# Kernel optimization log

Measured on AMD Instinct MI355X. Metric: run time of the kernel, lower is better.

Reference implementation:

```python
import jax, jax.numpy as jnp
import numpy as np


def _conv(x, w):
    # stride-2, pad-1, 3x3 conv, NCHW activations, HWIO kernel
    return jax.lax.conv_general_dilated(
        x, w, (2, 2), [(1, 1), (1, 1)],
        dimension_numbers=('NCHW', 'HWIO', 'NCHW'))


def setup_inputs() -> dict:
    key = jax.random.key(0)
    ks = iter(jax.random.split(key, 40))
    def rn(shape, scale=1.0):
        return jax.random.normal(next(ks), shape, jnp.float32) * scale
    d = {}
    d['img'] = rn((64, 3, 128, 128))
    d['qst'] = rn((64, 128))
    d['conv_w0'] = rn((3, 3, 3, 24), 1.0 / np.sqrt(3 * 9))
    for i in (1, 2, 3):
        d['conv_w%d' % i] = rn((3, 3, 24, 24), 1.0 / np.sqrt(24 * 9))
    for i in range(4):
        d['bn_s%d' % i] = jax.random.uniform(next(ks), (24,), jnp.float32, 0.5, 1.5)
        d['bn_b%d' % i] = rn((24,), 0.1)
    d['g_w1'] = rn((180, 256), 1.0 / np.sqrt(180))
    d['g_b1'] = rn((256,), 0.01)
    for i in (2, 3, 4):
        d['g_w%d' % i] = rn((256, 256), 1.0 / np.sqrt(256))
        d['g_b%d' % i] = rn((256,), 0.01)
    d['f_w1'] = rn((256, 256), 1.0 / np.sqrt(256))
    d['f_b1'] = rn((256,), 0.01)
    d['f_w2'] = rn((256, 256), 1.0 / np.sqrt(256))
    d['f_b2'] = rn((256,), 0.01)
    d['cls_w'] = rn((256, 32), 1.0 / np.sqrt(256))
    d['cls_b'] = rn((32,), 0.01)
    return d


def reference(img, qst, conv_w0, conv_w1, conv_w2, conv_w3,
              bn_s0, bn_b0, bn_s1, bn_b1, bn_s2, bn_b2, bn_s3, bn_b3,
              g_w1, g_b1, g_w2, g_b2, g_w3, g_b3, g_w4, g_b4,
              f_w1, f_b1, f_w2, f_b2, cls_w, cls_b):
    x = img
    for w, s, b in ((conv_w0, bn_s0, bn_b0), (conv_w1, bn_s1, bn_b1),
                    (conv_w2, bn_s2, bn_b2), (conv_w3, bn_s3, bn_b3)):
        x = jax.nn.relu(_conv(x, w) * s[None, :, None, None] + b[None, :, None, None])
    N, C, H, W = x.shape  # [64, 24, 8, 8]
    # positional encoding: coords_x, coords_y in [-1,1]
    cx, cy = jnp.meshgrid(jnp.linspace(-1.0, 1.0, W), jnp.linspace(-1.0, 1.0, H))
    pos = jnp.broadcast_to(jnp.stack([cx, cy])[None], (N, 2, H, W)).astype(x.dtype)
    x = jnp.concatenate([x, pos], axis=1)              # [N, C+2, H, W]
    Cf = C + 2
    x = x.transpose(0, 2, 3, 1).reshape(N, H * W, Cf)  # [N, HW, 26]
    # RN_G first linear decomposed over concat([x_i, x_j, qst]) so the huge
    # [N, HW, HW, 2C+q] concat tensor is never materialized (same math).
    W1a, W1b, W1c = g_w1[:Cf], g_w1[Cf:2 * Cf], g_w1[2 * Cf:]
    hi = x @ W1a                      # [N, HW, 256]
    hj = x @ W1b                      # [N, HW, 256]
    hq = qst @ W1c + g_b1             # [N, 256]
    h = jax.nn.relu(hi[:, :, None, :] + hj[:, None, :, :] + hq[:, None, None, :])  # [N,HW,HW,256]
    h = jax.nn.relu(h @ g_w2 + g_b2)
    h = jax.nn.relu(h @ g_w3 + g_b3)
    h = jax.nn.relu(h @ g_w4 + g_b4)
    s = h.sum(axis=(1, 2))            # sum over all HW*HW pairs -> [N, 256]
    # RN_F (dropout is identity in eval mode)
    y = jax.nn.relu(s @ f_w1 + f_b1)
    y = jax.nn.relu(y @ f_w2 + f_b2)
    return jax.nn.log_softmax(y @ cls_w + cls_b, axis=1)
```

## Files before the change

kernel.cpp:

```cpp
#include <hip/hip_runtime.h>
#include <hip/hip_bf16.h>
#include <math.h>

typedef __bf16 bf16x8 __attribute__((ext_vector_type(8)));
typedef __bf16 bf16x4 __attribute__((ext_vector_type(4)));
typedef float  f32x4  __attribute__((ext_vector_type(4)));

#define LH 264

__global__ __launch_bounds__(256) void k1(const float* __restrict__ img, const float* __restrict__ w0,
    const float* __restrict__ bs0, const float* __restrict__ bb0,
    const float* __restrict__ g2, const float* __restrict__ g3, const float* __restrict__ g4,
    const float* __restrict__ gw1, const float* __restrict__ gb1, const float* __restrict__ qst,
    float* __restrict__ c0, __bf16* __restrict__ Wt, float* __restrict__ hq,
    float* __restrict__ sbuf) {
  __shared__ __align__(16) float smem[8224];
  const int blk = blockIdx.x, t = threadIdx.x;

  if (blk < 512) {
    float* wl = smem;
    for (int i = t; i < 648; i += 256) wl[i] = w0[i];
    __syncthreads();
    const int H = 128, W = 128, OH = 64, OW = 64;
    int idx = blk * 256 + t;
    int oxh = idx & 31; int tt = idx >> 5; int oy = tt & 63; int n = tt >> 6;
    int ox0 = oxh * 2;
    float acc0[24], acc1[24];
#pragma unroll
    for (int co = 0; co < 24; ++co) { acc0[co] = 0.f; acc1[co] = 0.f; }
    for (int ci = 0; ci < 3; ++ci) {
      const float* xp = img + (size_t)(n * 3 + ci) * H * W;
#pragma unroll
      for (int ky = 0; ky < 3; ++ky) {
        int iy = 2 * oy + ky - 1;
        if (iy < 0 || iy >= H) continue;
        const float* row = xp + (size_t)iy * W;
        int ixb = 2 * ox0 - 1;
        float in[7];
#pragma unroll
        for (int u = 0; u < 7; ++u) {
          int ix = ixb + u;
          in[u] = (ix >= 0 && ix < W) ? row[ix] : 0.f;
        }
#pragma unroll
        for (int kx = 0; kx < 3; ++kx) {
          const float* wp = &wl[((ky * 3 + kx) * 3 + ci) * 24];
          float v0 = in[kx], v1 = in[kx + 2];
#pragma unroll
          for (int co = 0; co < 24; ++co) {
            float wv = wp[co];
            acc0[co] += v0 * wv;
            acc1[co] += v1 * wv;
          }
        }
      }
    }
    float* yp = c0 + (size_t)n * 24 * OH * OW + (size_t)oy * OW + ox0;
#pragma unroll
    for (int co = 0; co < 24; ++co) {
      float s = bs0[co], b = bb0[co];
      yp[(size_t)co * OH * OW]     = fmaxf(acc0[co] * s + b, 0.f);
      yp[(size_t)co * OH * OW + 1] = fmaxf(acc1[co] * s + b, 0.f);
    }
  } else if (blk < 536) {
    float* tile = smem;
    const int lb = blk - 512;
    const int l = lb >> 3, ks = lb & 7;
    const float* src = (l == 0) ? g2 : (l == 1) ? g3 : g4;
    for (int kk = 0; kk < 32; ++kk) tile[kk * 257 + t] = src[(ks * 32 + kk) * 256 + t];
    __syncthreads();
    const int q = t & 3, nb = t >> 2;
    __bf16* out = Wt + (size_t)(l * 8 + ks) * 8192;
#pragma unroll
    for (int i = 0; i < 4; ++i) {
      int nn = i * 64 + nb;
      bf16x8 v;
#pragma unroll
      for (int j = 0; j < 8; ++j) v[j] = (__bf16)tile[(q * 8 + j) * 257 + nn];
      *(bf16x8*)&out[nn * 32 + q * 8] = v;
    }
  } else {
    float* qs = smem;
    const int n = blk - 536;
    sbuf[n * 256 + t] = 0.f;
    if (t < 128) qs[t] = qst[n * 128 + t];
    __syncthreads();
    float a = gb1[t];
    for (int c = 0; c < 128; ++c) a += qs[c] * gw1[(52 + c) * 256 + t];
    hq[n * 256 + t] = a;
  }
}

__global__ __launch_bounds__(256) void conv1_k(const float* __restrict__ x, const float* __restrict__ w,
                                               const float* __restrict__ sc, const float* __restrict__ bi,
                                               float* __restrict__ y) {
  const int H = 64, W = 64, OH = 32, OW = 32;
  __shared__ float wl[2592];
  const int half = blockIdx.x & 1, sb = blockIdx.x >> 1;
  for (int i = threadIdx.x; i < 2592; i += 256) {
    int co = i % 12, rest = i / 12;
    wl[i] = w[rest * 24 + half * 12 + co];
  }
  __syncthreads();

  int idx = sb * 256 + threadIdx.x;
  int oxh = idx & 15; int tt = idx >> 4; int oy = tt & 31; int n = tt >> 5;
  int ox0 = oxh * 2;

  float acc0[12], acc1[12];
#pragma unroll
  for (int co = 0; co < 12; ++co) { acc0[co] = 0.f; acc1[co] = 0.f; }

  for (int ci = 0; ci < 24; ++ci) {
    const float* xp = x + (size_t)(n * 24 + ci) * H * W;
#pragma unroll
    for (int ky = 0; ky < 3; ++ky) {
      int iy = 2 * oy + ky - 1;
      if (iy < 0 || iy >= H) continue;
      const float* row = xp + (size_t)iy * W;
      int ixb = 2 * ox0 - 1;
      float in[7];
#pragma unroll
      for (int u = 0; u < 7; ++u) {
        int ix = ixb + u;
        in[u] = (ix >= 0 && ix < W) ? row[ix] : 0.f;
      }
#pragma unroll
      for (int kx = 0; kx < 3; ++kx) {
        const float* wp = &wl[((ky * 3 + kx) * 24 + ci) * 12];
        float v0 = in[kx], v1 = in[kx + 2];
#pragma unroll
        for (int co = 0; co < 12; ++co) {
          float wv = wp[co];
          acc0[co] += v0 * wv;
          acc1[co] += v1 * wv;
        }
      }
    }
  }
  float* yp = y + (size_t)n * 24 * OH * OW + (size_t)(half * 12) * OH * OW + (size_t)oy * OW + ox0;
#pragma unroll
  for (int co = 0; co < 12; ++co) {
    int cog = half * 12 + co;
    float s = sc[cog], b = bi[cog];
    yp[(size_t)co * OH * OW]     = fmaxf(acc0[co] * s + b, 0.f);
    yp[(size_t)co * OH * OW + 1] = fmaxf(acc1[co] * s + b, 0.f);
  }
}

__global__ __launch_bounds__(256) void chain2_k(const float* __restrict__ c1,
    const float* __restrict__ w2, const float* __restrict__ bs2, const float* __restrict__ bb2,
    const float* __restrict__ w3, const float* __restrict__ bs3, const float* __restrict__ bb3,
    const float* __restrict__ gw1, float* __restrict__ hi, float* __restrict__ hj) {
  __shared__ float sw[5184];
  __shared__ float s2[6144];
  __shared__ float s3[1536];
  const int n = blockIdx.x, t = threadIdx.x;
  for (int i = t; i < 5184; i += 256) sw[i] = w2[i];
  __syncthreads();
  {
    int ox = t & 15, oy = t >> 4;
    float acc[24];
#pragma unroll
    for (int co = 0; co < 24; ++co) acc[co] = 0.f;
    for (int ci = 0; ci < 24; ++ci) {
      const float* xp = c1 + (size_t)(n * 24 + ci) * 1024;
#pragma unroll
      for (int ky = 0; ky < 3; ++ky) {
        int iy = 2 * oy + ky - 1;
        if (iy < 0 || iy >= 32) continue;
#pragma unroll
        for (int kx = 0; kx < 3; ++kx) {
          int ix = 2 * ox + kx - 1;
          if (ix < 0 || ix >= 32) continue;
          float v = xp[iy * 32 + ix];
          const float* wp = &sw[((ky * 3 + kx) * 24 + ci) * 24];
#pragma unroll
          for (int co = 0; co < 24; ++co) acc[co] += v * wp[co];
        }
      }
    }
#pragma unroll
    for (int co = 0; co < 24; ++co)
      s2[co * 256 + t] = fmaxf(acc[co] * bs2[co] + bb2[co], 0.f);
  }
  __syncthreads();
  for (int i = t; i < 5184; i += 256) sw[i] = w3[i];
  __syncthreads();
  {
    const int pos = t & 63, cog = t >> 6;
    const int oy = pos >> 3, ox = pos & 7;
    float acc[6];
#pragma unroll
    for (int u = 0; u < 6; ++u) acc[u] = 0.f;
    for (int ci = 0; ci < 24; ++ci) {
      const float* cp = &s2[ci * 256];
#pragma unroll
      for (int ky = 0; ky < 3; ++ky) {
        int iy = 2 * oy + ky - 1;
        if (iy < 0 || iy >= 16) continue;
#pragma unroll
        for (int kx = 0; kx < 3; ++kx) {
          int ix = 2 * ox + kx - 1;
          if (ix < 0 || ix >= 16) continue;
          float v = cp[iy * 16 + ix];
          const float* wp = &sw[((ky * 3 + kx) * 24 + ci) * 24 + cog * 6];
#pragma unroll
          for (int u = 0; u < 6; ++u) acc[u] += v * wp[u];
        }
      }
    }
#pragma unroll
    for (int u = 0; u < 6; ++u) {
      int co = cog * 6 + u;
      s3[co * 64 + pos] = fmaxf(acc[u] * bs3[co] + bb3[co], 0.f);
    }
  }
  float wa[26], wb[26];
#pragma unroll
  for (int c = 0; c < 26; ++c) {
    wa[c] = gw1[c * 256 + t];
    wb[c] = gw1[(26 + c) * 256 + t];
  }
  __syncthreads();
  for (int p = 0; p < 64; ++p) {
    float a = 0.f, b = 0.f;
#pragma unroll
    for (int c = 0; c < 24; ++c) {
      float v = s3[c * 64 + p];
      a += v * wa[c];
      b += v * wb[c];
    }
    float cx = -1.f + (2.f / 7.f) * (float)(p & 7);
    float cy = -1.f + (2.f / 7.f) * (float)(p >> 3);
    a += cx * wa[24] + cy * wa[25];
    b += cx * wb[24] + cy * wb[25];
    hi[(size_t)(n * 64 + p) * 256 + t] = a;
    hj[(size_t)(n * 64 + p) * 256 + t] = b;
  }
}

__global__ __launch_bounds__(256, 2)
void g_fused(const float* __restrict__ hi, const float* __restrict__ hj,
             const float* __restrict__ hq, const __bf16* __restrict__ Wt,
             const float* __restrict__ b2, const float* __restrict__ b3,
             const float* __restrict__ b4, float* __restrict__ s_out) {
  const int blk = blockIdx.x;
  const int n = blk >> 5, ib = blk & 31;
  const int tid = threadIdx.x;
  const int wave = tid >> 6, lane = tid & 63;
  const int q = lane >> 4, lr = lane & 15;

  __shared__ __align__(16) __bf16 Hs[128 * LH];

  const int c0 = (tid & 63) * 4;
  float4 hq4 = *(const float4*)(hq + (size_t)n * 256 + c0);
  float4 h0 = *(const float4*)(hi + (size_t)(n * 64 + ib * 2)     * 256 + c0);
  float4 h1 = *(const float4*)(hi + (size_t)(n * 64 + ib * 2 + 1) * 256 + c0);
  h0.x += hq4.x; h0.y += hq4.y; h0.z += hq4.z; h0.w += hq4.w;
  h1.x += hq4.x; h1.y += hq4.y; h1.z += hq4.z; h1.w += hq4.w;

  const int colloc = wave * 64 + lr;
  float bias[3][4];
#pragma unroll
  for (int c = 0; c < 4; ++c) {
    bias[0][c] = b2[colloc + c * 16];
    bias[1][c] = b3[colloc + c * 16];
    bias[2][c] = b4[colloc + c * 16];
  }

  const float* hjb = hj + (size_t)n * 64 * 256;
#pragma unroll
  for (int it = 0; it < 16; ++it) {
    int j = it * 4 + wave;
    float4 v = *(const float4*)(hjb + j * 256 + c0);
    bf16x4 o;
    o[0] = (__bf16)fmaxf(v.x + h0.x, 0.f);
    o[1] = (__bf16)fmaxf(v.y + h0.y, 0.f);
    o[2] = (__bf16)fmaxf(v.z + h0.z, 0.f);
    o[3] = (__bf16)fmaxf(v.w + h0.w, 0.f);
    *(bf16x4*)&Hs[j * LH + c0] = o;
    bf16x4 o2;
    o2[0] = (__bf16)fmaxf(v.x + h1.x, 0.f);
    o2[1] = (__bf16)fmaxf(v.y + h1.y, 0.f);
    o2[2] = (__bf16)fmaxf(v.z + h1.z, 0.f);
    o2[3] = (__bf16)fmaxf(v.w + h1.w, 0.f);
    *(bf16x4*)&Hs[(64 + j) * LH + c0] = o2;
  }
  __syncthreads();

  const __bf16* Bp = Wt + (size_t)wave * 2048 + lr * 32 + q * 8;

  for (int l = 0; l < 3; ++l) {
    const __bf16* Bl = Bp + (size_t)l * 65536;

    f32x4 acc[8][4];
#pragma unroll
    for (int r = 0; r < 8; ++r)
#pragma unroll
      for (int c = 0; c < 4; ++c) acc[r][c] = (f32x4){0.f, 0.f, 0.f, 0.f};

    for (int ks = 0; ks < 8; ++ks) {
      bf16x8 b[4];
#pragma unroll
      for (int c = 0; c < 4; ++c)
        b[c] = *(const bf16x8*)&Bl[ks * 8192 + c * 512];
      bf16x8 a[8];
#pragma unroll
      for (int r = 0; r < 8; ++r)
        a[r] = *(const bf16x8*)&Hs[(r * 16 + lr) * LH + ks * 32 + q * 8];
#pragma unroll
      for (int r = 0; r < 8; ++r)
#pragma unroll
        for (int c = 0; c < 4; ++c)
          acc[r][c] = __builtin_amdgcn_mfma_f32_16x16x32_bf16(a[r], b[c], acc[r][c], 0, 0, 0);
    }

    if (l < 2) {
      __syncthreads();
#pragma unroll
      for (int r = 0; r < 8; ++r)
#pragma unroll
        for (int c = 0; c < 4; ++c)
#pragma unroll
          for (int reg = 0; reg < 4; ++reg) {
            int row = r * 16 + q * 4 + reg;
            Hs[row * LH + colloc + c * 16] = (__bf16)fmaxf(acc[r][c][reg] + bias[l][c], 0.f);
          }
      __syncthreads();
    } else {
#pragma unroll
      for (int c = 0; c < 4; ++c) {
        float cs = 0.f;
#pragma unroll
        for (int r = 0; r < 8; ++r)
#pragma unroll
          for (int reg = 0; reg < 4; ++reg)
            cs += fmaxf(acc[r][c][reg] + bias[2][c], 0.f);
        cs += __shfl_xor(cs, 16);
        cs += __shfl_xor(cs, 32);
        if (q == 0) atomicAdd(&s_out[n * 256 + colloc + c * 16], cs);
      }
    }
  }
}

__global__ void f_net(const float* __restrict__ s, const float* __restrict__ fw1,
                      const float* __restrict__ fb1, const float* __restrict__ fw2,
                      const float* __restrict__ fb2, const float* __restrict__ cw,
                      const float* __restrict__ cb, float* __restrict__ out) {
  int n = blockIdx.x, t = threadIdx.x;
  __shared__ float buf[256], buf2[256], zs[32];
  buf[t] = s[n * 256 + t];
  __syncthreads();
  float a = fb1[t];
  for (int c = 0; c < 256; ++c) a += buf[c] * fw1[c * 256 + t];
  a = fmaxf(a, 0.f);
  buf2[t] = a;
  __syncthreads();
  float y = fb2[t];
  for (int c = 0; c < 256; ++c) y += buf2[c] * fw2[c * 256 + t];
  y = fmaxf(y, 0.f);
  __syncthreads();
  buf[t] = y;
  __syncthreads();
  float z = 0.f;
  if (t < 32) {
    z = cb[t];
    for (int c = 0; c < 256; ++c) z += buf[c] * cw[c * 32 + t];
    zs[t] = z;
  }
  __syncthreads();
  if (t < 32) {
    float m = -1e30f;
    for (int c = 0; c < 32; ++c) m = fmaxf(m, zs[c]);
    float se = 0.f;
    for (int c = 0; c < 32; ++c) se += expf(zs[c] - m);
    out[n * 32 + t] = z - m - logf(se);
  }
}

extern "C" void kernel_launch(void* const* d_in, const int* in_sizes, int n_in,
                              void* d_out, int out_size, void* d_ws, size_t ws_size,
                              hipStream_t stream) {
  const float* img  = (const float*)d_in[0];
  const float* qst  = (const float*)d_in[1];
  const float* w0   = (const float*)d_in[2];
  const float* w1   = (const float*)d_in[3];
  const float* w2   = (const float*)d_in[4];
  const float* w3   = (const float*)d_in[5];
  const float* bs0  = (const float*)d_in[6];
  const float* bb0  = (const float*)d_in[7];
  const float* bs1  = (const float*)d_in[8];
  const float* bb1  = (const float*)d_in[9];
  const float* bs2  = (const float*)d_in[10];
  const float* bb2  = (const float*)d_in[11];
  const float* bs3  = (const float*)d_in[12];
  const float* bb3  = (const float*)d_in[13];
  const float* gw1  = (const float*)d_in[14];
  const float* gb1  = (const float*)d_in[15];
  const float* gw2  = (const float*)d_in[16];
  const float* gb2  = (const float*)d_in[17];
  const float* gw3  = (const float*)d_in[18];
  const float* gb3  = (const float*)d_in[19];
  const float* gw4  = (const float*)d_in[20];
  const float* gb4  = (const float*)d_in[21];
  const float* fw1  = (const float*)d_in[22];
  const float* fb1  = (const float*)d_in[23];
  const float* fw2  = (const float*)d_in[24];
  const float* fb2  = (const float*)d_in[25];
  const float* cw   = (const float*)d_in[26];
  const float* cb   = (const float*)d_in[27];

  char* ws = (char*)d_ws;
  float* c0 = (float*)(ws + 0);
  float* c1 = (float*)(ws + 25165824);
  __bf16* Wt  = (__bf16*)(ws + 31457280);
  float*  hqb = (float*)(ws + 31850496);
  float*  sbuf = (float*)(ws + 31916032);
  float*  hi  = (float*)(ws + 0);
  float*  hj  = (float*)(ws + 4194304);

  k1<<<600, 256, 0, stream>>>(img, w0, bs0, bb0, gw2, gw3, gw4, gw1, gb1, qst,
                              c0, Wt, hqb, sbuf);
  conv1_k<<<256, 256, 0, stream>>>(c0, w1, bs1, bb1, c1);
  chain2_k<<<64, 256, 0, stream>>>(c1, w2, bs2, bb2, w3, bs3, bb3, gw1, hi, hj);
  g_fused<<<2048, 256, 0, stream>>>(hi, hj, hqb, Wt, gb2, gb3, gb4, sbuf);
  f_net<<<64, 256, 0, stream>>>(sbuf, fw1, fb1, fw2, fb2, cw, cb, (float*)d_out);
}
```

Before: 313.9 us.

## Permute weight columns and swap MFMA operands for vectorized LDS writeback

The weight-prep block now permutes output columns of the first two G layers. In g_fused, those layers swap the MFMA A/B operands so each lane holds contiguous output columns, allowing 16-byte bf16x8 stores back to shared memory instead of scalar bf16 stores. The initial pair-construction stage also writes 8 bf16 per thread. The goal is fewer and wider LDS writes between layers, at the cost of a permuted weight layout that must stay consistent with the permuted activation channel order.

After: 308.9 us. Within noise of the previous version (-1.6%).

```diff
diff --git a/kernel.cpp b/kernel.cpp
--- a/kernel.cpp
+++ b/kernel.cpp
@@ -7,6 +7,10 @@
 typedef float  f32x4  __attribute__((ext_vector_type(4)));
 
 #define LH 264
+
+__device__ __host__ inline int fperm(int p) {
+  return (p & 0xC0) | ((p & 0x0C) << 2) | ((p >> 2) & 0x0C) | (p & 3);
+}
 
 __global__ __launch_bounds__(256) void k1(const float* __restrict__ img, const float* __restrict__ w0,
     const float* __restrict__ bs0, const float* __restrict__ bb0,
@@ -74,9 +78,10 @@
 #pragma unroll
     for (int i = 0; i < 4; ++i) {
       int nn = i * 64 + nb;
+      int fsel = (l < 2) ? fperm(nn) : nn;
       bf16x8 v;
 #pragma unroll
-      for (int j = 0; j < 8; ++j) v[j] = (__bf16)tile[(q * 8 + j) * 257 + nn];
+      for (int j = 0; j < 8; ++j) v[j] = (__bf16)tile[(q * 8 + j) * 257 + fsel];
       *(bf16x8*)&out[nn * 32 + q * 8] = v;
     }
   } else {
@@ -253,46 +258,49 @@
 
   __shared__ __align__(16) __bf16 Hs[128 * LH];
 
-  const int c0 = (tid & 63) * 4;
-  float4 hq4 = *(const float4*)(hq + (size_t)n * 256 + c0);
-  float4 h0 = *(const float4*)(hi + (size_t)(n * 64 + ib * 2)     * 256 + c0);
-  float4 h1 = *(const float4*)(hi + (size_t)(n * 64 + ib * 2 + 1) * 256 + c0);
-  h0.x += hq4.x; h0.y += hq4.y; h0.z += hq4.z; h0.w += hq4.w;
-  h1.x += hq4.x; h1.y += hq4.y; h1.z += hq4.z; h1.w += hq4.w;
-
-  const int colloc = wave * 64 + lr;
-  float bias[3][4];
-#pragma unroll
-  for (int c = 0; c < 4; ++c) {
-    bias[0][c] = b2[colloc + c * 16];
-    bias[1][c] = b3[colloc + c * 16];
-    bias[2][c] = b4[colloc + c * 16];
-  }
+  const int half = lane >> 5, m = lane & 31;
+  const int cb = m * 8;
+  float4 hqA = *(const float4*)(hq + (size_t)n * 256 + cb);
+  float4 hqB = *(const float4*)(hq + (size_t)n * 256 + cb + 4);
+  float4 hiA = *(const float4*)(hi + (size_t)(n * 64 + ib * 2 + half) * 256 + cb);
+  float4 hiB = *(const float4*)(hi + (size_t)(n * 64 + ib * 2 + half) * 256 + cb + 4);
+  float hh[8];
+  hh[0] = hiA.x + hqA.x; hh[1] = hiA.y + hqA.y; hh[2] = hiA.z + hqA.z; hh[3] = hiA.w + hqA.w;
+  hh[4] = hiB.x + hqB.x; hh[5] = hiB.y + hqB.y; hh[6] = hiB.z + hqB.z; hh[7] = hiB.w + hqB.w;
+
+  float bias2[4];
+#pragma unroll
+  for (int c = 0; c < 4; ++c) bias2[c] = b4[wave * 64 + lr + c * 16];
 
   const float* hjb = hj + (size_t)n * 64 * 256;
 #pragma unroll
   for (int it = 0; it < 16; ++it) {
     int j = it * 4 + wave;
-    float4 v = *(const float4*)(hjb + j * 256 + c0);
-    bf16x4 o;
-    o[0] = (__bf16)fmaxf(v.x + h0.x, 0.f);
-    o[1] = (__bf16)fmaxf(v.y + h0.y, 0.f);
-    o[2] = (__bf16)fmaxf(v.z + h0.z, 0.f);
-    o[3] = (__bf16)fmaxf(v.w + h0.w, 0.f);
-    *(bf16x4*)&Hs[j * LH + c0] = o;
-    bf16x4 o2;
-    o2[0] = (__bf16)fmaxf(v.x + h1.x, 0.f);
-    o2[1] = (__bf16)fmaxf(v.y + h1.y, 0.f);
-    o2[2] = (__bf16)fmaxf(v.z + h1.z, 0.f);
-    o2[3] = (__bf16)fmaxf(v.w + h1.w, 0.f);
-    *(bf16x4*)&Hs[(64 + j) * LH + c0] = o2;
+    float4 va = *(const float4*)(hjb + j * 256 + cb);
+    float4 vb = *(const float4*)(hjb + j * 256 + cb + 4);
+    bf16x8 o;
+    o[0] = (__bf16)fmaxf(va.x + hh[0], 0.f);
+    o[1] = (__bf16)fmaxf(va.y + hh[1], 0.f);
+    o[2] = (__bf16)fmaxf(va.z + hh[2], 0.f);
+    o[3] = (__bf16)fmaxf(va.w + hh[3], 0.f);
+    o[4] = (__bf16)fmaxf(vb.x + hh[4], 0.f);
+    o[5] = (__bf16)fmaxf(vb.y + hh[5], 0.f);
+    o[6] = (__bf16)fmaxf(vb.z + hh[6], 0.f);
+    o[7] = (__bf16)fmaxf(vb.w + hh[7], 0.f);
+    *(bf16x8*)&Hs[(size_t)(half * 64 + j) * LH + cb] = o;
   }
   __syncthreads();
 
   const __bf16* Bp = Wt + (size_t)wave * 2048 + lr * 32 + q * 8;
-
-  for (int l = 0; l < 3; ++l) {
+  const int colv = wave * 64 + q * 16;
+
+  for (int l = 0; l < 2; ++l) {
     const __bf16* Bl = Bp + (size_t)l * 65536;
+    const float* bb = (l == 0) ? b2 : b3;
+    f32x4 bv[4];
+#pragma unroll
+    for (int c = 0; c < 4; ++c)
+      bv[c] = *(const f32x4*)(bb + colv + c * 4);
 
     f32x4 acc[8][4];
 #pragma unroll
@@ -308,7 +316,52 @@
       bf16x8 a[8];
 #pragma unroll
       for (int r = 0; r < 8; ++r)
-        a[r] = *(const bf16x8*)&Hs[(r * 16 + lr) * LH + ks * 32 + q * 8];
+        a[r] = *(const bf16x8*)&Hs[(size_t)(r * 16 + lr) * LH + ks * 32 + q * 8];
+#pragma unroll
+      for (int r = 0; r < 8; ++r)
+#pragma unroll
+        for (int c = 0; c < 4; ++c)
+          acc[r][c] = __builtin_amdgcn_mfma_f32_16x16x32_bf16(b[c], a[r], acc[r][c], 0, 0, 0);
+    }
+
+    __syncthreads();
+#pragma unroll
+    for (int r = 0; r < 8; ++r) {
+      bf16x8 oA, oB;
+#pragma unroll
+      for (int c = 0; c < 2; ++c)
+#pragma unroll
+        for (int reg = 0; reg < 4; ++reg)
+          oA[c * 4 + reg] = (__bf16)fmaxf(acc[r][c][reg] + bv[c][reg], 0.f);
+#pragma unroll
+      for (int c = 2; c < 4; ++c)
+#pragma unroll
+        for (int reg = 0; reg < 4; ++reg)
+          oB[(c - 2) * 4 + reg] = (__bf16)fmaxf(acc[r][c][reg] + bv[c][reg], 0.f);
+      __bf16* wp = &Hs[(size_t)(r * 16 + lr) * LH + colv];
+      *(bf16x8*)wp = oA;
+      *(bf16x8*)(wp + 8) = oB;
+    }
+    __syncthreads();
+  }
+
+  {
+    const __bf16* Bl = Bp + (size_t)2 * 65536;
+    f32x4 acc[8][4];
+#pragma unroll
+    for (int r = 0; r < 8; ++r)
+#pragma unroll
+      for (int c = 0; c < 4; ++c) acc[r][c] = (f32x4){0.f, 0.f, 0.f, 0.f};
+
+    for (int ks = 0; ks < 8; ++ks) {
+      bf16x8 b[4];
+#pragma unroll
+      for (int c = 0; c < 4; ++c)
+        b[c] = *(const bf16x8*)&Bl[ks * 8192 + c * 512];
+      bf16x8 a[8];
+#pragma unroll
+      for (int r = 0; r < 8; ++r)
+        a[r] = *(const bf16x8*)&Hs[(size_t)(r * 16 + lr) * LH + ks * 32 + q * 8];
 #pragma unroll
       for (int r = 0; r < 8; ++r)
 #pragma unroll
@@ -316,31 +369,17 @@
           acc[r][c] = __builtin_amdgcn_mfma_f32_16x16x32_bf16(a[r], b[c], acc[r][c], 0, 0, 0);
     }
 
-    if (l < 2) {
-      __syncthreads();
+#pragma unroll
+    for (int c = 0; c < 4; ++c) {
+      float cs = 0.f;
 #pragma unroll
       for (int r = 0; r < 8; ++r)
 #pragma unroll
-        for (int c = 0; c < 4; ++c)
-#pragma unroll
-          for (int reg = 0; reg < 4; ++reg) {
-            int row = r * 16 + q * 4 + reg;
-            Hs[row * LH + colloc + c * 16] = (__bf16)fmaxf(acc[r][c][reg] + bias[l][c], 0.f);
-          }
-      __syncthreads();
-    } else {
-#pragma unroll
-      for (int c = 0; c < 4; ++c) {
-        float cs = 0.f;
-#pragma unroll
-        for (int r = 0; r < 8; ++r)
-#pragma unroll
-          for (int reg = 0; reg < 4; ++reg)
-            cs += fmaxf(acc[r][c][reg] + bias[2][c], 0.f);
-        cs += __shfl_xor(cs, 16);
-        cs += __shfl_xor(cs, 32);
-        if (q == 0) atomicAdd(&s_out[n * 256 + colloc + c * 16], cs);
-      }
+        for (int reg = 0; reg < 4; ++reg)
+          cs += fmaxf(acc[r][c][reg] + bias2[c], 0.f);
+      cs += __shfl_xor(cs, 16);
+      cs += __shfl_xor(cs, 32);
+      if (q == 0) atomicAdd(&s_out[n * 256 + wave * 64 + lr + c * 16], cs);
     }
   }
 }
```
